# Performance work log

Hardware: AMD Instinct MI355X
Metric: run time of the kernel (lower is better)

## Reference

```python
import jax, jax.numpy as jnp
import numpy as np

D_MODEL = 256
N_HEAD = 8
D_FF = 1024
B = 8
N_PER = 4096
NQ = B * N_PER
L = 16
NEG_INF = -1e9
EPS = 1e-5


def layer_norm(x, g, b):
    mu = jnp.mean(x, axis=-1, keepdims=True)
    var = jnp.mean(jnp.square(x - mu), axis=-1, keepdims=True)
    return (x - mu) * jax.lax.rsqrt(var + EPS) * g + b


def setup_inputs() -> dict:
    key = jax.random.key(0)
    ks = jax.random.split(key, 20)
    s = 1.0 / np.sqrt(D_MODEL)
    sf = 1.0 / np.sqrt(D_FF)
    inp = {
        "src": jax.random.normal(ks[0], (NQ, D_MODEL), jnp.float32),
        "pos": jax.random.normal(ks[1], (NQ, D_MODEL), jnp.float32),
        # per-batch-relative neighbor indices in [-1, N_PER); -1 == invalid/padded
        "index_pair": jax.random.randint(ks[2], (NQ, L), 0, N_PER + 1, jnp.int32) - 1,
        "query_batch_cnt": jnp.full((B,), N_PER, jnp.int32),
        "key_batch_cnt": jnp.full((B,), N_PER, jnp.int32),
        "index_pair_batch": (jnp.arange(NQ, dtype=jnp.int32) // N_PER).astype(jnp.int32),
        "Wq": jax.random.normal(ks[3], (D_MODEL, D_MODEL), jnp.float32) * s,
        "bq": jnp.zeros((D_MODEL,), jnp.float32),
        "Wk": jax.random.normal(ks[4], (D_MODEL, D_MODEL), jnp.float32) * s,
        "bk": jnp.zeros((D_MODEL,), jnp.float32),
        "Wv": jax.random.normal(ks[5], (D_MODEL, D_MODEL), jnp.float32) * s,
        "bv": jnp.zeros((D_MODEL,), jnp.float32),
        "Wo": jax.random.normal(ks[6], (D_MODEL, D_MODEL), jnp.float32) * s,
        "bo": jnp.zeros((D_MODEL,), jnp.float32),
        "W1": jax.random.normal(ks[7], (D_MODEL, D_FF), jnp.float32) * s,
        "b1": jnp.zeros((D_FF,), jnp.float32),
        "W2": jax.random.normal(ks[8], (D_FF, D_MODEL), jnp.float32) * sf,
        "b2": jnp.zeros((D_MODEL,), jnp.float32),
        "g1": jnp.ones((D_MODEL,), jnp.float32),
        "be1": jnp.zeros((D_MODEL,), jnp.float32),
        "g2": jnp.ones((D_MODEL,), jnp.float32),
        "be2": jnp.zeros((D_MODEL,), jnp.float32),
    }
    return inp


def local_attn(q, k, v, index_pair, key_batch_cnt, index_pair_batch,
               Wq, bq, Wk, bk, Wv, bv, Wo, bo):
    H, hd = N_HEAD, D_MODEL // N_HEAD
    scale = 1.0 / np.sqrt(hd)
    qh = (q @ Wq + bq).reshape(NQ, H, hd) * scale        # [Nq,H,hd]
    kh = (k @ Wk + bk).reshape(NQ, H, hd)                # [Nk,H,hd] (Nk==Nq)
    vh = (v @ Wv + bv).reshape(NQ, H, hd)
    # start offset of each batch's keys in the stacked key tensor
    offs = jnp.cumsum(key_batch_cnt) - key_batch_cnt      # [B]
    valid = index_pair >= 0                               # [Nq,L]
    gidx = jnp.where(valid, index_pair + offs[index_pair_batch][:, None], 0)
    k_g = kh[gidx]                                        # [Nq,L,H,hd]
    v_g = vh[gidx]                                        # [Nq,L,H,hd]
    logits = jnp.einsum('nhd,nlhd->nhl', qh, k_g)         # [Nq,H,L]
    logits = jnp.where(valid[:, None, :], logits, NEG_INF)
    attn = jax.nn.softmax(logits, axis=-1)
    out = jnp.einsum('nhl,nlhd->nhd', attn, v_g).reshape(NQ, D_MODEL)
    return out @ Wo + bo


def reference(src, pos, index_pair, query_batch_cnt, key_batch_cnt, index_pair_batch,
              Wq, bq, Wk, bk, Wv, bv, Wo, bo, W1, b1, W2, b2, g1, be1, g2, be2):
    # forward_post (normalize_before=False), dropout==0 (eval)
    qk = src + pos
    src2 = local_attn(qk, qk, src, index_pair, key_batch_cnt, index_pair_batch,
                      Wq, bq, Wk, bk, Wv, bv, Wo, bo)
    x = layer_norm(src + src2, g1, be1)
    ff = jax.nn.relu(x @ W1 + b1) @ W2 + b2
    return layer_norm(x + ff, g2, be2)
```

## Files before the change

kernel.cpp:

```cpp
#include <hip/hip_runtime.h>
#include <hip/hip_bf16.h>
#include <cstdint>
#include <cstddef>

#define NQ_ 32768
#define DM_ 256
#define DFF_ 1024
#define LNB_ 16
#define NB_ 8

typedef __attribute__((ext_vector_type(4))) float f32x4;
typedef __attribute__((ext_vector_type(8))) short s16x8;

__device__ __forceinline__ float bf2f(ushort u) {
    union { unsigned int i; float f; } c; c.i = ((unsigned int)u) << 16; return c.f;
}
__device__ __forceinline__ ushort f2bf(float f) {
    union { float f; unsigned int i; } c; c.f = f;
    unsigned int x = c.i;
    return (ushort)((x + 0x7fffu + ((x >> 16) & 1u)) >> 16);
}


__global__ __launch_bounds__(256) void prep_qk(const float* __restrict__ src, const float* __restrict__ pos,
                                               ushort* __restrict__ qkb, ushort* __restrict__ srcb) {
    int i = (blockIdx.x * 256 + threadIdx.x) * 4;
    float4 s = *(const float4*)(src + i);
    float4 p = *(const float4*)(pos + i);
    ushort4 a, b;
    a.x = f2bf(s.x + p.x); a.y = f2bf(s.y + p.y); a.z = f2bf(s.z + p.z); a.w = f2bf(s.w + p.w);
    b.x = f2bf(s.x);       b.y = f2bf(s.y);       b.z = f2bf(s.z);       b.w = f2bf(s.w);
    *(ushort4*)(qkb + i) = a;
    *(ushort4*)(srcb + i) = b;
}

__global__ __launch_bounds__(256) void prep_weights(const float* __restrict__ Wq, const float* __restrict__ Wk,
                                                    const float* __restrict__ Wv, const float* __restrict__ Wo,
                                                    const float* __restrict__ W1, const float* __restrict__ W2,
                                                    const int* __restrict__ kbc,
                                                    const float* __restrict__ bq, const float* __restrict__ bk,
                                                    ushort* __restrict__ WqT, ushort* __restrict__ WkT,
                                                    ushort* __restrict__ WvT, ushort* __restrict__ WoT,
                                                    ushort* __restrict__ W1T, ushort* __restrict__ W2T,
                                                    int* __restrict__ offs, float* __restrict__ bias2) {
    const int b = blockIdx.x;
    const int t = threadIdx.x;
    if (b == 3072) {
        if (t == 0) { int a = 0; for (int i = 0; i < NB_; ++i) { offs[i] = a; a += kbc[i]; } }
        bias2[t] = bq[t];
        bias2[256 + t] = bk[t];
        return;
    }
    const float* W; ushort* Wt; int base, ks, ns;
    if (b < 1024) {
        const int sec = b >> 8;
        W  = sec == 0 ? Wq  : sec == 1 ? Wk  : sec == 2 ? Wv  : Wo;
        Wt = sec == 0 ? WqT : sec == 1 ? WkT : sec == 2 ? WvT : WoT;
        base = (b & 255) * 256; ks = 8; ns = 8;
    } else if (b < 2048) {
        W = W1; Wt = W1T; base = (b - 1024) * 256; ks = 8; ns = 10;
    } else {
        W = W2; Wt = W2T; base = (b - 2048) * 256; ks = 10; ns = 8;
    }
    const int i = base + t;
    const int n = i >> ks, k = i & ((1 << ks) - 1);
    Wt[i] = f2bf(W[(k << ns) + n]);
}


__device__ __forceinline__ void gld_lds16(const ushort* g, ushort* l) {
    __builtin_amdgcn_global_load_lds((const __attribute__((address_space(1))) void*)g,
                                     (__attribute__((address_space(3))) void*)l, 16, 0, 0);
}

template <bool RELU>
__global__ __launch_bounds__(256) void gemm_kernel(const ushort* __restrict__ A, const ushort* __restrict__ Bt,
                                                   const float* __restrict__ bias, ushort* __restrict__ C,
                                                   int M, int N, int K, float alpha) {
    __shared__ __align__(16) ushort As[2 * 128 * 32];
    __shared__ __align__(16) ushort Bs[2 * 128 * 32];
    const int tid = threadIdx.x;
    const int lane = tid & 63;
    const int wave = tid >> 6;
    const int wr = wave >> 1, wc = wave & 1;
    const long m0 = (long)blockIdx.x * 128;
    const long n0 = (long)blockIdx.y * 128;

    f32x4 acc[4][4] = {};

    const int c0 = tid, c1 = tid + 256;
    const int ar0 = c0 >> 2, ac0 = c0 & 3;
    const int ar1 = c1 >> 2, ac1 = c1 & 3;
    const int as0 = (ac0 ^ ((ar0 >> 1) & 3)) * 8;
    const int as1 = (ac1 ^ ((ar1 >> 1) & 3)) * 8;
    const int la = lane & 15;
    const int sx = ((lane >> 4) ^ ((la >> 1) & 3)) * 8;

    const ushort* Ar0 = A + (m0 + ar0) * K + as0;
    const ushort* Ar1 = A + (m0 + ar1) * K + as1;
    const ushort* Br0 = Bt + (n0 + ar0) * K + as0;
    const ushort* Br1 = Bt + (n0 + ar1) * K + as1;

    const int nt = K >> 5;
    int boff = 0;
    gld_lds16(Ar0, As + c0 * 8);
    gld_lds16(Ar1, As + c1 * 8);
    gld_lds16(Br0, Bs + c0 * 8);
    gld_lds16(Br1, Bs + c1 * 8);

    for (int t = 0; t < nt; ++t) {
        if (t + 1 < nt) {
            const int kt = (t + 1) << 5;
            const int nb = boff ^ 4096;
            gld_lds16(Ar0 + kt, As + nb + c0 * 8);
            gld_lds16(Ar1 + kt, As + nb + c1 * 8);
            gld_lds16(Br0 + kt, Bs + nb + c0 * 8);
            gld_lds16(Br1 + kt, Bs + nb + c1 * 8);
            asm volatile("s_waitcnt vmcnt(4)" ::: "memory");
        } else {
            asm volatile("s_waitcnt vmcnt(0)" ::: "memory");
        }
        __builtin_amdgcn_s_barrier();
        s16x8 af[4], bfr[4];
#pragma unroll
        for (int m = 0; m < 4; ++m)
            af[m] = *(const s16x8*)(As + boff + (wr * 64 + m * 16 + la) * 32 + sx);
#pragma unroll
        for (int n = 0; n < 4; ++n)
            bfr[n] = *(const s16x8*)(Bs + boff + (wc * 64 + n * 16 + la) * 32 + sx);
        asm volatile("s_waitcnt lgkmcnt(0)" ::: "memory");
        __builtin_amdgcn_s_barrier();
#pragma unroll
        for (int m = 0; m < 4; ++m)
#pragma unroll
            for (int n = 0; n < 4; ++n)
                acc[m][n] = __builtin_amdgcn_mfma_f32_16x16x32_bf16(af[m], bfr[n], acc[m][n], 0, 0, 0);
        boff ^= 4096;
    }

#pragma unroll
    for (int n = 0; n < 4; ++n) {
        const long col = n0 + wc * 64 + n * 16 + la;
        const float bv = bias[col];
#pragma unroll
        for (int m = 0; m < 4; ++m) {
#pragma unroll
            for (int j = 0; j < 4; ++j) {
                const long row = m0 + wr * 64 + m * 16 + (lane >> 4) * 4 + j;
                float r = (acc[m][n][j] + bv) * alpha;
                if (RELU) r = fmaxf(r, 0.f);
                C[row * N + col] = f2bf(r);
            }
        }
    }
}


__global__ __launch_bounds__(256, 4) void attn_kernel(const ushort* __restrict__ QKb,
                                                      const ushort* __restrict__ Vb, const int* __restrict__ ipair,
                                                      const int* __restrict__ ipb, const int* __restrict__ offs,
                                                      ushort* __restrict__ Ob) {
    const int blk = (blockIdx.x & 7) * (NQ_ / 16 / 8) + (blockIdx.x >> 3);
    const int lane = threadIdx.x & 63;
    const int n = blk * 16 + (threadIdx.x >> 6) * 4 + (lane >> 4);
    const size_t hoff = (size_t)(lane & 15) * 16;

    float q[16];
    {
        const ushort* qr = QKb + (size_t)n * 512 + hoff;
#pragma unroll
        for (int c = 0; c < 2; ++c) {
            s16x8 v = *(const s16x8*)(qr + c * 8);
#pragma unroll
            for (int e = 0; e < 8; ++e) q[c * 8 + e] = bf2f((ushort)v[e]);
        }
    }
    const int off = offs[ipb[n]];
    int gi[LNB_];
    float lg[LNB_];
#pragma unroll
    for (int j = 0; j < LNB_; ++j) {
        const int ip = ipair[n * LNB_ + j];
        const int g = ip >= 0 ? ip + off : 0;
        gi[j] = g;
        const ushort* kr = QKb + (size_t)g * 512 + 256 + hoff;
        float p = 0.f;
#pragma unroll
        for (int c = 0; c < 2; ++c) {
            s16x8 v = *(const s16x8*)(kr + c * 8);
#pragma unroll
            for (int e = 0; e < 8; ++e)
                p = fmaf(q[c * 8 + e], bf2f((ushort)v[e]), p);
        }
        p += __shfl_xor(p, 1);
        lg[j] = ip >= 0 ? p * 0.17677669529663688f : -1e9f;
    }
    float mx = lg[0];
#pragma unroll
    for (int j = 1; j < LNB_; ++j) mx = fmaxf(mx, lg[j]);
    float sum = 0.f, pw[LNB_];
#pragma unroll
    for (int j = 0; j < LNB_; ++j) { pw[j] = __expf(lg[j] - mx); sum += pw[j]; }
    const float inv = 1.f / sum;

    float acc[16] = {};
#pragma unroll
    for (int j = 0; j < LNB_; ++j) {
        const ushort* vr = Vb + (size_t)gi[j] * DM_ + hoff;
        const float w = pw[j] * inv;
#pragma unroll
        for (int c = 0; c < 2; ++c) {
            s16x8 v = *(const s16x8*)(vr + c * 8);
#pragma unroll
            for (int e = 0; e < 8; ++e)
                acc[c * 8 + e] = fmaf(w, bf2f((ushort)v[e]), acc[c * 8 + e]);
        }
    }
    ushort* orow = Ob + (size_t)n * DM_ + hoff;
#pragma unroll
    for (int c = 0; c < 2; ++c) {
        s16x8 o;
#pragma unroll
        for (int e = 0; e < 8; ++e) o[e] = (short)f2bf(acc[c * 8 + e]);
        *(s16x8*)(orow + c * 8) = o;
    }
}


__global__ __launch_bounds__(256) void ln1_kernel(const ushort* __restrict__ a, const ushort* __restrict__ y,
                                                  const float* __restrict__ g, const float* __restrict__ be,
                                                  ushort* __restrict__ out) {
    const int row = blockIdx.x * 4 + (threadIdx.x >> 6);
    const int lane = threadIdx.x & 63;
    const int e = lane * 4;
    const size_t base = (size_t)row * DM_ + e;
    ushort4 av = *(const ushort4*)(a + base);
    ushort4 yv = *(const ushort4*)(y + base);
    float v0 = bf2f(av.x) + bf2f(yv.x), v1 = bf2f(av.y) + bf2f(yv.y);
    float v2 = bf2f(av.z) + bf2f(yv.z), v3 = bf2f(av.w) + bf2f(yv.w);
    float s = v0 + v1 + v2 + v3;
#pragma unroll
    for (int mk = 1; mk < 64; mk <<= 1) s += __shfl_xor(s, mk);
    const float mu = s * (1.f / 256.f);
    v0 -= mu; v1 -= mu; v2 -= mu; v3 -= mu;
    float qv = v0 * v0 + v1 * v1 + v2 * v2 + v3 * v3;
#pragma unroll
    for (int mk = 1; mk < 64; mk <<= 1) qv += __shfl_xor(qv, mk);
    const float r = rsqrtf(qv * (1.f / 256.f) + 1e-5f);
    ushort4 o;
    o.x = f2bf(v0 * r * g[e] + be[e]);
    o.y = f2bf(v1 * r * g[e + 1] + be[e + 1]);
    o.z = f2bf(v2 * r * g[e + 2] + be[e + 2]);
    o.w = f2bf(v3 * r * g[e + 3] + be[e + 3]);
    *(ushort4*)(out + base) = o;
}

__global__ __launch_bounds__(256) void ln2_kernel(const ushort* __restrict__ x, const ushort* __restrict__ f,
                                                  const float* __restrict__ g, const float* __restrict__ be,
                                                  float* __restrict__ out) {
    const int row = blockIdx.x * 4 + (threadIdx.x >> 6);
    const int lane = threadIdx.x & 63;
    const int e = lane * 4;
    const size_t base = (size_t)row * DM_ + e;
    ushort4 xv = *(const ushort4*)(x + base);
    ushort4 fv = *(const ushort4*)(f + base);
    float v0 = bf2f(xv.x) + bf2f(fv.x), v1 = bf2f(xv.y) + bf2f(fv.y);
    float v2 = bf2f(xv.z) + bf2f(fv.z), v3 = bf2f(xv.w) + bf2f(fv.w);
    float s = v0 + v1 + v2 + v3;
#pragma unroll
    for (int mk = 1; mk < 64; mk <<= 1) s += __shfl_xor(s, mk);
    const float mu = s * (1.f / 256.f);
    v0 -= mu; v1 -= mu; v2 -= mu; v3 -= mu;
    float qv = v0 * v0 + v1 * v1 + v2 * v2 + v3 * v3;
#pragma unroll
    for (int mk = 1; mk < 64; mk <<= 1) qv += __shfl_xor(qv, mk);
    const float r = rsqrtf(qv * (1.f / 256.f) + 1e-5f);
    float4 o;
    o.x = v0 * r * g[e] + be[e];
    o.y = v1 * r * g[e + 1] + be[e + 1];
    o.z = v2 * r * g[e + 2] + be[e + 2];
    o.w = v3 * r * g[e + 3] + be[e + 3];
    *(float4*)(out + base) = o;
}


extern "C" void kernel_launch(void* const* d_in, const int* in_sizes, int n_in,
                              void* d_out, int out_size, void* d_ws, size_t ws_size,
                              hipStream_t stream) {
    const float* src = (const float*)d_in[0];
    const float* pos = (const float*)d_in[1];
    const int* ipair = (const int*)d_in[2];
    const int* kbc   = (const int*)d_in[4];
    const int* ipb   = (const int*)d_in[5];
    const float* Wq = (const float*)d_in[6];  const float* bq = (const float*)d_in[7];
    const float* Wk = (const float*)d_in[8];  const float* bk = (const float*)d_in[9];
    const float* Wv = (const float*)d_in[10]; const float* bv = (const float*)d_in[11];
    const float* Wo = (const float*)d_in[12]; const float* bo = (const float*)d_in[13];
    const float* W1 = (const float*)d_in[14]; const float* b1 = (const float*)d_in[15];
    const float* W2 = (const float*)d_in[16]; const float* b2 = (const float*)d_in[17];
    const float* g1 = (const float*)d_in[18]; const float* be1 = (const float*)d_in[19];
    const float* g2 = (const float*)d_in[20]; const float* be2 = (const float*)d_in[21];

    char* ws = (char*)d_ws;
    const size_t SB = (size_t)NQ_ * DM_ * 2;
    ushort* qkb  = (ushort*)(ws);
    ushort* srcb = (ushort*)(ws + SB);
    ushort* QKb  = (ushort*)(ws + 2 * SB);
    ushort* Vb   = (ushort*)(ws + 4 * SB);
    ushort* fb   = (ushort*)(ws + 5 * SB);
    ushort* hb   = (ushort*)(ws);
    ushort* attno = qkb;
    ushort* yb    = (ushort*)(ws + 2 * SB);
    ushort* xb    = Vb;
    char* wb = ws + 6 * SB;
    ushort* WqT = (ushort*)(wb);
    ushort* WkT = (ushort*)(wb + 131072);
    ushort* WvT = (ushort*)(wb + 262144);
    ushort* WoT = (ushort*)(wb + 393216);
    ushort* W1T = (ushort*)(wb + 524288);
    ushort* W2T = (ushort*)(wb + 1048576);
    int* offs   = (int*)(wb + 1572864);
    float* bias2 = (float*)(wb + 1572864 + 64);

    prep_weights<<<3073, 256, 0, stream>>>(Wq, Wk, Wv, Wo, W1, W2, kbc, bq, bk,
                                           WqT, WkT, WvT, WoT, W1T, W2T, offs, bias2);
    prep_qk<<<NQ_ * DM_ / 4 / 256, 256, 0, stream>>>(src, pos, qkb, srcb);

    dim3 gqk(NQ_ / 128, 512 / 128);
    dim3 g256(NQ_ / 128, DM_ / 128);
    dim3 gff1(NQ_ / 128, DFF_ / 128);
    gemm_kernel<false><<<gqk, 256, 0, stream>>>(qkb, WqT, bias2, QKb, NQ_, 512, DM_, 1.f);
    gemm_kernel<false><<<g256, 256, 0, stream>>>(srcb, WvT, bv, Vb, NQ_, DM_, DM_, 1.f);
    attn_kernel<<<NQ_ / 16, 256, 0, stream>>>(QKb, Vb, ipair, ipb, offs, attno);
    gemm_kernel<false><<<g256, 256, 0, stream>>>(attno, WoT, bo, yb, NQ_, DM_, DM_, 1.f);
    ln1_kernel<<<NQ_ / 4, 256, 0, stream>>>(srcb, yb, g1, be1, xb);
    gemm_kernel<true><<<gff1, 256, 0, stream>>>(xb, W1T, b1, hb, NQ_, DFF_, DM_, 1.f);
    gemm_kernel<false><<<g256, 256, 0, stream>>>(hb, W2T, b2, fb, NQ_, DM_, DFF_, 1.f);
    ln2_kernel<<<NQ_ / 4, 256, 0, stream>>>(xb, fb, g2, be2, (float*)d_out);
}
```

Measured before the change: 196.0 us.

## Remap GEMM tiles across XCDs and halve per-thread work in attention

```diff
diff --git a/kernel.cpp b/kernel.cpp
--- a/kernel.cpp
+++ b/kernel.cpp
@@ -83,8 +83,13 @@
     const int lane = tid & 63;
     const int wave = tid >> 6;
     const int wr = wave >> 1, wc = wave & 1;
-    const long m0 = (long)blockIdx.x * 128;
-    const long n0 = (long)blockIdx.y * 128;
+
+    const int b = (int)(blockIdx.y * gridDim.x + blockIdx.x);
+    const int idx = b >> 3;
+    const int xt = (b & 7) * 32 + (idx & 31);
+    const int yt = idx >> 5;
+    const long m0 = (long)xt * 128;
+    const long n0 = (long)yt * 128;
 
     f32x4 acc[4][4] = {};
 
@@ -160,20 +165,16 @@
                                                       const ushort* __restrict__ Vb, const int* __restrict__ ipair,
                                                       const int* __restrict__ ipb, const int* __restrict__ offs,
                                                       ushort* __restrict__ Ob) {
-    const int blk = (blockIdx.x & 7) * (NQ_ / 16 / 8) + (blockIdx.x >> 3);
+    const int blk = (blockIdx.x & 7) * (NQ_ / 8 / 8) + (blockIdx.x >> 3);
     const int lane = threadIdx.x & 63;
-    const int n = blk * 16 + (threadIdx.x >> 6) * 4 + (lane >> 4);
-    const size_t hoff = (size_t)(lane & 15) * 16;
-
-    float q[16];
+    const int n = blk * 8 + (threadIdx.x >> 6) * 2 + (lane >> 5);
+    const size_t hoff = (size_t)(lane & 31) * 8;
+
+    float q[8];
     {
-        const ushort* qr = QKb + (size_t)n * 512 + hoff;
-#pragma unroll
-        for (int c = 0; c < 2; ++c) {
-            s16x8 v = *(const s16x8*)(qr + c * 8);
-#pragma unroll
-            for (int e = 0; e < 8; ++e) q[c * 8 + e] = bf2f((ushort)v[e]);
-        }
+        s16x8 v = *(const s16x8*)(QKb + (size_t)n * 512 + hoff);
+#pragma unroll
+        for (int e = 0; e < 8; ++e) q[e] = bf2f((ushort)v[e]);
     }
     const int off = offs[ipb[n]];
     int gi[LNB_];
@@ -183,16 +184,13 @@
         const int ip = ipair[n * LNB_ + j];
         const int g = ip >= 0 ? ip + off : 0;
         gi[j] = g;
-        const ushort* kr = QKb + (size_t)g * 512 + 256 + hoff;
+        s16x8 v = *(const s16x8*)(QKb + (size_t)g * 512 + 256 + hoff);
         float p = 0.f;
 #pragma unroll
-        for (int c = 0; c < 2; ++c) {
-            s16x8 v = *(const s16x8*)(kr + c * 8);
-#pragma unroll
-            for (int e = 0; e < 8; ++e)
-                p = fmaf(q[c * 8 + e], bf2f((ushort)v[e]), p);
-        }
+        for (int e = 0; e < 8; ++e)
+            p = fmaf(q[e], bf2f((ushort)v[e]), p);
         p += __shfl_xor(p, 1);
+        p += __shfl_xor(p, 2);
         lg[j] = ip >= 0 ? p * 0.17677669529663688f : -1e9f;
     }
     float mx = lg[0];
@@ -203,27 +201,19 @@
     for (int j = 0; j < LNB_; ++j) { pw[j] = __expf(lg[j] - mx); sum += pw[j]; }
     const float inv = 1.f / sum;
 
-    float acc[16] = {};
+    float acc[8] = {};
 #pragma unroll
     for (int j = 0; j < LNB_; ++j) {
-        const ushort* vr = Vb + (size_t)gi[j] * DM_ + hoff;
+        s16x8 v = *(const s16x8*)(Vb + (size_t)gi[j] * DM_ + hoff);
         const float w = pw[j] * inv;
 #pragma unroll
-        for (int c = 0; c < 2; ++c) {
-            s16x8 v = *(const s16x8*)(vr + c * 8);
-#pragma unroll
-            for (int e = 0; e < 8; ++e)
-                acc[c * 8 + e] = fmaf(w, bf2f((ushort)v[e]), acc[c * 8 + e]);
-        }
-    }
-    ushort* orow = Ob + (size_t)n * DM_ + hoff;
-#pragma unroll
-    for (int c = 0; c < 2; ++c) {
-        s16x8 o;
-#pragma unroll
-        for (int e = 0; e < 8; ++e) o[e] = (short)f2bf(acc[c * 8 + e]);
-        *(s16x8*)(orow + c * 8) = o;
-    }
+        for (int e = 0; e < 8; ++e)
+            acc[e] = fmaf(w, bf2f((ushort)v[e]), acc[e]);
+    }
+    s16x8 o;
+#pragma unroll
+    for (int e = 0; e < 8; ++e) o[e] = (short)f2bf(acc[e]);
+    *(s16x8*)(Ob + (size_t)n * DM_ + hoff) = o;
 }
 
 
@@ -331,7 +321,7 @@
     dim3 gff1(NQ_ / 128, DFF_ / 128);
     gemm_kernel<false><<<gqk, 256, 0, stream>>>(qkb, WqT, bias2, QKb, NQ_, 512, DM_, 1.f);
     gemm_kernel<false><<<g256, 256, 0, stream>>>(srcb, WvT, bv, Vb, NQ_, DM_, DM_, 1.f);
-    attn_kernel<<<NQ_ / 16, 256, 0, stream>>>(QKb, Vb, ipair, ipb, offs, attno);
+    attn_kernel<<<NQ_ / 8, 256, 0, stream>>>(QKb, Vb, ipair, ipb, offs, attno);
     gemm_kernel<false><<<g256, 256, 0, stream>>>(attno, WoT, bo, yb, NQ_, DM_, DM_, 1.f);
     ln1_kernel<<<NQ_ / 4, 256, 0, stream>>>(srcb, yb, g1, be1, xb);
     gemm_kernel<true><<<gff1, 256, 0, stream>>>(xb, W1T, b1, hb, NQ_, DFF_, DM_, 1.f);
```

Measured after the change: 184.6 us. 1.06x faster.
